# Performance work log

Hardware: AMD Instinct MI355X
Metric: run time of the kernel (lower is better)

Reference implementation:

```python
import jax, jax.numpy as jnp
import numpy as np

N = 100000
K = 16
C_IN = 64
C_MID = 64   # max(in_channels, out_channels // 2)
C_OUT = 128
EPS = 1e-5


def setup_inputs() -> dict:
    key = jax.random.key(0)
    ks = jax.random.split(key, 4)
    feat = jax.random.normal(ks[0], (N, C_IN), dtype=jnp.float32)
    reference_index = jax.random.randint(ks[1], (N, K), 0, N, dtype=jnp.int64)
    # Kaiming-ish init for the two Linear layers (torch Linear default scale)
    W1 = jax.random.normal(ks[2], (C_IN, C_MID), dtype=jnp.float32) / np.sqrt(C_IN)
    W2 = jax.random.normal(ks[3], (C_MID, C_OUT), dtype=jnp.float32) / np.sqrt(C_MID)
    return {
        "feat": feat,
        "reference_index": reference_index,
        "W1": W1,
        "b1": jnp.zeros((C_MID,), jnp.float32),
        "gamma1": jnp.ones((C_MID,), jnp.float32),
        "beta1": jnp.zeros((C_MID,), jnp.float32),
        "W2": W2,
        "b2": jnp.zeros((C_OUT,), jnp.float32),
        "gamma2": jnp.ones((C_OUT,), jnp.float32),
        "beta2": jnp.zeros((C_OUT,), jnp.float32),
    }


def _bn(x, gamma, beta):
    # BatchNorm1d in training mode: biased batch stats over the row dim.
    mean = jnp.mean(x, axis=0)
    var = jnp.var(x, axis=0)
    return (x - mean) * jax.lax.rsqrt(var + EPS) * gamma + beta


def reference(feat, reference_index, W1, b1, gamma1, beta1, W2, b2, gamma2, beta2):
    # grouping (with_xyz=False): gather neighbor features -> [N, K, C_IN]
    grouped = feat[reference_index]
    x = grouped.reshape(-1, C_IN)                 # [N*K, C_IN]
    h = jax.nn.relu(_bn(x @ W1 + b1, gamma1, beta1))   # [N*K, C_MID]
    h = jax.nn.relu(_bn(h @ W2 + b2, gamma2, beta2))   # [N*K, C_OUT]
    out = h.reshape(N, K, C_OUT).max(axis=1)      # max-pool over neighbors
    return out
```

## Files before the change

### kernel.cpp

```cpp
#include <hip/hip_runtime.h>
#include <hip/hip_bf16.h>

#define N_PTS 100000
#define KNN   16
#define NK    (N_PTS * KNN)
#define CIN   64
#define CMID  64
#define COUT  128

#define HSLC    64
#define SEG_CNT 25000
#define SEG_U32 12500

#define OFF_Z2B   0
#define OFF_Z1B   25600000
#define OFF_CNT   38400000
#define OFF_STATS 38800000
#define OFF_W2BF  38801536
#define OFF_W1BF  38817920

typedef __attribute__((ext_vector_type(8))) short bf16x8;
typedef __attribute__((ext_vector_type(4))) float f32x4;
union U8 { uint4 u; bf16x8 v; unsigned short s[8]; };

__device__ __forceinline__ unsigned short f2bf(float f) {
    unsigned u = __float_as_uint(f);
    unsigned r = (u + 0x7fffu + ((u >> 16) & 1u)) >> 16;
    return (unsigned short)r;
}

__global__ __launch_bounds__(256) void hist_k(const int* __restrict__ idx,
                                              unsigned short* __restrict__ pc) {
    __shared__ unsigned int smem[SEG_U32];
    int seg  = blockIdx.x & 3;
    int slc  = blockIdx.x >> 2;
    int base = seg * SEG_CNT;

    for (int i = threadIdx.x; i < SEG_U32; i += 256) smem[i] = 0;
    __syncthreads();

    const int4* ip = (const int4*)idx;
    const int per = NK / 4 / HSLC;
    int s = slc * per, e = s + per;
    for (int i = s + threadIdx.x; i < e; i += 256) {
        int4 v = ip[i];
        int a;
        a = v.x - base; if ((unsigned)a < (unsigned)SEG_CNT)
            atomicAdd(&smem[a >> 1], 1u << ((a & 1) * 16));
        a = v.y - base; if ((unsigned)a < (unsigned)SEG_CNT)
            atomicAdd(&smem[a >> 1], 1u << ((a & 1) * 16));
        a = v.z - base; if ((unsigned)a < (unsigned)SEG_CNT)
            atomicAdd(&smem[a >> 1], 1u << ((a & 1) * 16));
        a = v.w - base; if ((unsigned)a < (unsigned)SEG_CNT)
            atomicAdd(&smem[a >> 1], 1u << ((a & 1) * 16));
    }
    __syncthreads();

    unsigned int* outp = (unsigned int*)(pc + (size_t)slc * N_PTS) + seg * SEG_U32;
    for (int i = threadIdx.x; i < SEG_U32; i += 256) outp[i] = smem[i];
}

__global__ __launch_bounds__(256) void sum_counts_k(const unsigned short* __restrict__ pc,
                                                    float* __restrict__ counts,
                                                    const float* __restrict__ W2,
                                                    unsigned short* __restrict__ w2bf,
                                                    const float* __restrict__ W1,
                                                    unsigned short* __restrict__ w1bf) {
    if (blockIdx.x == 196) {
        for (int e = threadIdx.x; e < 8192; e += 256) {
            int j = e & 7, lane = (e >> 3) & 63, kh = (e >> 9) & 1, nt = e >> 10;
            int k = kh * 32 + (lane >> 4) * 8 + j;
            int n = nt * 16 + (lane & 15);
            w2bf[e] = f2bf(W2[k * COUT + n]);
        }
        return;
    }
    if (blockIdx.x == 197) {
        for (int e = threadIdx.x; e < 4096; e += 256) {
            int j = e & 7, lane = (e >> 3) & 63, kh = (e >> 9) & 1, nt = e >> 10;
            int k = kh * 32 + (lane >> 4) * 8 + j;
            int n = nt * 16 + (lane & 15);
            w1bf[e] = f2bf(W1[k * CMID + n]);
        }
        return;
    }
    int i = blockIdx.x * 256 + threadIdx.x;
    if (i >= N_PTS / 2) return;
    const unsigned int* p = (const unsigned int*)pc;
    unsigned int u = 0;
    #pragma unroll
    for (int s = 0; s < HSLC; s++) u += p[s * (N_PTS / 2) + i];
    float2 r;
    r.x = (float)(u & 0xffffu);
    r.y = (float)(u >> 16);
    ((float2*)counts)[i] = r;
}

__global__ __launch_bounds__(256) void gemm1_k(const float* __restrict__ feat,
                                               const unsigned short* __restrict__ w1bf,
                                               const float* __restrict__ b1,
                                               const float* __restrict__ counts,
                                               unsigned short* __restrict__ z1b,
                                               float* __restrict__ S1,
                                               float* __restrict__ Q1) {
    int lane = threadIdx.x & 63, wid = threadIdx.x >> 6;
    int il = lane & 15, quad = lane >> 4;

    bf16x8 wf[4][2];
    const uint4* wp = (const uint4*)w1bf;
    #pragma unroll
    for (int nt = 0; nt < 4; nt++) {
        U8 t0; t0.u = wp[(nt * 2 + 0) * 64 + lane]; wf[nt][0] = t0.v;
        U8 t1; t1.u = wp[(nt * 2 + 1) * 64 + lane]; wf[nt][1] = t1.v;
    }
    float bias[4];
    #pragma unroll
    for (int nt = 0; nt < 4; nt++) bias[nt] = b1[nt * 16 + il];

    float s[4] = {0, 0, 0, 0}, q[4] = {0, 0, 0, 0};

    int wgid = blockIdx.x * 4 + wid;
    for (int tile = wgid; tile < N_PTS / 16; tile += gridDim.x * 4) {
        int m0 = tile * 16;
        const float* fr = feat + (size_t)(m0 + il) * 64;
        float4 fa = *(const float4*)(fr + quad * 8);
        float4 fb = *(const float4*)(fr + quad * 8 + 4);
        float4 fc = *(const float4*)(fr + 32 + quad * 8);
        float4 fd = *(const float4*)(fr + 32 + quad * 8 + 4);
        U8 ua, ub;
        ua.s[0] = f2bf(fa.x); ua.s[1] = f2bf(fa.y); ua.s[2] = f2bf(fa.z); ua.s[3] = f2bf(fa.w);
        ua.s[4] = f2bf(fb.x); ua.s[5] = f2bf(fb.y); ua.s[6] = f2bf(fb.z); ua.s[7] = f2bf(fb.w);
        ub.s[0] = f2bf(fc.x); ub.s[1] = f2bf(fc.y); ub.s[2] = f2bf(fc.z); ub.s[3] = f2bf(fc.w);
        ub.s[4] = f2bf(fd.x); ub.s[5] = f2bf(fd.y); ub.s[6] = f2bf(fd.z); ub.s[7] = f2bf(fd.w);

        float4 cnt4 = *(const float4*)(counts + m0 + quad * 4);
        #pragma unroll
        for (int nt = 0; nt < 4; nt++) {
            f32x4 acc = {bias[nt], bias[nt], bias[nt], bias[nt]};
            acc = __builtin_amdgcn_mfma_f32_16x16x32_bf16(ua.v, wf[nt][0], acc, 0, 0, 0);
            acc = __builtin_amdgcn_mfma_f32_16x16x32_bf16(ub.v, wf[nt][1], acc, 0, 0, 0);
            unsigned short* zp = z1b + (size_t)(m0 + quad * 4) * 64 + nt * 16 + il;
            zp[0]   = f2bf(acc[0]);
            zp[64]  = f2bf(acc[1]);
            zp[128] = f2bf(acc[2]);
            zp[192] = f2bf(acc[3]);
            s[nt] += cnt4.x * acc[0] + cnt4.y * acc[1] + cnt4.z * acc[2] + cnt4.w * acc[3];
            q[nt] += cnt4.x * acc[0] * acc[0] + cnt4.y * acc[1] * acc[1]
                   + cnt4.z * acc[2] * acc[2] + cnt4.w * acc[3] * acc[3];
        }
    }
    #pragma unroll
    for (int m = 16; m <= 32; m <<= 1) {
        #pragma unroll
        for (int nt = 0; nt < 4; nt++) {
            s[nt] += __shfl_xor(s[nt], m, 64);
            q[nt] += __shfl_xor(q[nt], m, 64);
        }
    }
    __shared__ float sred[2][4][4][16];
    if (quad == 0) {
        #pragma unroll
        for (int nt = 0; nt < 4; nt++) { sred[0][wid][nt][il] = s[nt]; sred[1][wid][nt][il] = q[nt]; }
    }
    __syncthreads();
    if (threadIdx.x < 128) {
        int which = threadIdx.x >> 6, c = threadIdx.x & 63;
        float t = sred[which][0][c >> 4][c & 15] + sred[which][1][c >> 4][c & 15]
                + sred[which][2][c >> 4][c & 15] + sred[which][3][c >> 4][c & 15];
        atomicAdd(which ? &Q1[c] : &S1[c], t);
    }
}

__device__ __forceinline__ bf16x8 bnrelu(uint4 r, float4 alo, float4 ahi,
                                         float4 blo, float4 bhi) {
    float z0 = __uint_as_float(r.x << 16), z1 = __uint_as_float(r.x & 0xffff0000u);
    float z2 = __uint_as_float(r.y << 16), z3 = __uint_as_float(r.y & 0xffff0000u);
    float z4 = __uint_as_float(r.z << 16), z5 = __uint_as_float(r.z & 0xffff0000u);
    float z6 = __uint_as_float(r.w << 16), z7 = __uint_as_float(r.w & 0xffff0000u);
    U8 o;
    o.s[0] = f2bf(fmaxf(fmaf(alo.x, z0, blo.x), 0.f));
    o.s[1] = f2bf(fmaxf(fmaf(alo.y, z1, blo.y), 0.f));
    o.s[2] = f2bf(fmaxf(fmaf(alo.z, z2, blo.z), 0.f));
    o.s[3] = f2bf(fmaxf(fmaf(alo.w, z3, blo.w), 0.f));
    o.s[4] = f2bf(fmaxf(fmaf(ahi.x, z4, bhi.x), 0.f));
    o.s[5] = f2bf(fmaxf(fmaf(ahi.y, z5, bhi.y), 0.f));
    o.s[6] = f2bf(fmaxf(fmaf(ahi.z, z6, bhi.z), 0.f));
    o.s[7] = f2bf(fmaxf(fmaf(ahi.w, z7, bhi.w), 0.f));
    return o.v;
}

__global__ __launch_bounds__(256) void gemm2_k(const unsigned short* __restrict__ z1b,
                                               const unsigned short* __restrict__ w2bf,
                                               const float* __restrict__ S1,
                                               const float* __restrict__ Q1,
                                               const float* __restrict__ g1,
                                               const float* __restrict__ be1,
                                               const float* __restrict__ b2,
                                               const float* __restrict__ counts,
                                               unsigned short* __restrict__ z2b,
                                               float* __restrict__ S2,
                                               float* __restrict__ Q2) {
    __shared__ float Al[64], Bl[64];
    if (threadIdx.x < 64) {
        const float inv = 1.0f / (float)NK;
        float m = S1[threadIdx.x] * inv;
        float v = Q1[threadIdx.x] * inv - m * m;
        float a = g1[threadIdx.x] * rsqrtf(v + 1e-5f);
        Al[threadIdx.x] = a;
        Bl[threadIdx.x] = be1[threadIdx.x] - m * a;
    }
    __syncthreads();

    int lane = threadIdx.x & 63, wid = threadIdx.x >> 6;
    int il = lane & 15, quad = lane >> 4;

    float4 a0lo = *(const float4*)(Al + quad * 8);
    float4 a0hi = *(const float4*)(Al + quad * 8 + 4);
    float4 b0lo = *(const float4*)(Bl + quad * 8);
    float4 b0hi = *(const float4*)(Bl + quad * 8 + 4);
    float4 a1lo = *(const float4*)(Al + 32 + quad * 8);
    float4 a1hi = *(const float4*)(Al + 32 + quad * 8 + 4);
    float4 b1lo = *(const float4*)(Bl + 32 + quad * 8);
    float4 b1hi = *(const float4*)(Bl + 32 + quad * 8 + 4);

    bf16x8 bfr[8][2];
    const uint4* wp = (const uint4*)w2bf;
    #pragma unroll
    for (int nt = 0; nt < 8; nt++) {
        U8 t0; t0.u = wp[(nt * 2 + 0) * 64 + lane]; bfr[nt][0] = t0.v;
        U8 t1; t1.u = wp[(nt * 2 + 1) * 64 + lane]; bfr[nt][1] = t1.v;
    }
    float bias[8];
    #pragma unroll
    for (int nt = 0; nt < 8; nt++) bias[nt] = b2[nt * 16 + il];

    float s[8], q[8];
    #pragma unroll
    for (int j = 0; j < 8; j++) { s[j] = 0.f; q[j] = 0.f; }

    int wgid = blockIdx.x * 4 + wid;
    for (int tile = wgid; tile < N_PTS / 16; tile += gridDim.x * 4) {
        int m0 = tile * 16;
        const uint4* ar = (const uint4*)(z1b + (size_t)(m0 + il) * 64);
        uint4 ra0 = ar[quad];
        uint4 ra1 = ar[4 + quad];
        bf16x8 af0 = bnrelu(ra0, a0lo, a0hi, b0lo, b0hi);
        bf16x8 af1 = bnrelu(ra1, a1lo, a1hi, b1lo, b1hi);
        float4 cnt4 = *(const float4*)(counts + m0 + quad * 4);
        #pragma unroll
        for (int nt = 0; nt < 8; nt++) {
            f32x4 acc = {bias[nt], bias[nt], bias[nt], bias[nt]};
            acc = __builtin_amdgcn_mfma_f32_16x16x32_bf16(af0, bfr[nt][0], acc, 0, 0, 0);
            acc = __builtin_amdgcn_mfma_f32_16x16x32_bf16(af1, bfr[nt][1], acc, 0, 0, 0);
            unsigned short* zp = z2b + ((size_t)(nt >> 2) * N_PTS + m0 + quad * 4) * 64
                                     + (nt & 3) * 16 + il;
            zp[0]   = f2bf(acc[0]);
            zp[64]  = f2bf(acc[1]);
            zp[128] = f2bf(acc[2]);
            zp[192] = f2bf(acc[3]);
            s[nt] += cnt4.x * acc[0] + cnt4.y * acc[1] + cnt4.z * acc[2] + cnt4.w * acc[3];
            q[nt] += cnt4.x * acc[0] * acc[0] + cnt4.y * acc[1] * acc[1]
                   + cnt4.z * acc[2] * acc[2] + cnt4.w * acc[3] * acc[3];
        }
    }
    #pragma unroll
    for (int m = 16; m <= 32; m <<= 1) {
        #pragma unroll
        for (int nt = 0; nt < 8; nt++) {
            s[nt] += __shfl_xor(s[nt], m, 64);
            q[nt] += __shfl_xor(q[nt], m, 64);
        }
    }
    __shared__ float sred[2][4][8][16];
    if (quad == 0) {
        #pragma unroll
        for (int nt = 0; nt < 8; nt++) { sred[0][wid][nt][il] = s[nt]; sred[1][wid][nt][il] = q[nt]; }
    }
    __syncthreads();
    {
        int which = threadIdx.x >> 7, c = threadIdx.x & 127;
        float t = sred[which][0][c >> 4][c & 15] + sred[which][1][c >> 4][c & 15]
                + sred[which][2][c >> 4][c & 15] + sred[which][3][c >> 4][c & 15];
        atomicAdd(which ? &Q2[c] : &S2[c], t);
    }
}

__global__ __launch_bounds__(256) void gather_k(const unsigned int* __restrict__ z2u,
                                                const int* __restrict__ idx,
                                                const float* __restrict__ S2,
                                                const float* __restrict__ Q2,
                                                const float* __restrict__ g2,
                                                const float* __restrict__ be2,
                                                float* __restrict__ out) {
    int lane = threadIdx.x & 63, wid = threadIdx.x >> 6;
    int half = blockIdx.x / (N_PTS / 8);
    int n    = (blockIdx.x % (N_PTS / 8)) * 8 + wid * 2 + (lane >> 5);
    int sl   = lane & 31;

    const float inv = 1.0f / (float)NK;
    float2 Sv = ((const float2*)S2)[half * 32 + sl];
    float2 Qv = ((const float2*)Q2)[half * 32 + sl];
    float2 gv = ((const float2*)g2)[half * 32 + sl];
    float2 bv = ((const float2*)be2)[half * 32 + sl];
    float m0c = Sv.x * inv, m1c = Sv.y * inv;
    float a0 = gv.x * rsqrtf(Qv.x * inv - m0c * m0c + 1e-5f);
    float a1 = gv.y * rsqrtf(Qv.y * inv - m1c * m1c + 1e-5f);
    float b0 = bv.x - m0c * a0;
    float b1 = bv.y - m1c * a1;

    const int* ip = idx + n * KNN;
    const unsigned int* zh = z2u + (size_t)half * N_PTS * 32;
    float mx0 = -1e30f, mn0 = 1e30f, mx1 = -1e30f, mn1 = 1e30f;
    #pragma unroll
    for (int k = 0; k < KNN; k++) {
        int j = ip[k];
        unsigned v = zh[(size_t)j * 32 + sl];
        float f0 = __uint_as_float(v << 16);
        float f1 = __uint_as_float(v & 0xffff0000u);
        mx0 = fmaxf(mx0, f0); mn0 = fminf(mn0, f0);
        mx1 = fmaxf(mx1, f1); mn1 = fminf(mn1, f1);
    }
    float2 r;
    r.x = fmaxf(fmaxf(fmaf(a0, mx0, b0), fmaf(a0, mn0, b0)), 0.f);
    r.y = fmaxf(fmaxf(fmaf(a1, mx1, b1), fmaf(a1, mn1, b1)), 0.f);
    ((float2*)(out + (size_t)n * COUT + half * 64))[sl] = r;
}

extern "C" void kernel_launch(void* const* d_in, const int* in_sizes, int n_in,
                              void* d_out, int out_size, void* d_ws, size_t ws_size,
                              hipStream_t stream) {
    const float* feat = (const float*)d_in[0];
    const int*   idx  = (const int*)d_in[1];
    const float* W1   = (const float*)d_in[2];
    const float* b1   = (const float*)d_in[3];
    const float* g1   = (const float*)d_in[4];
    const float* be1  = (const float*)d_in[5];
    const float* W2   = (const float*)d_in[6];
    const float* b2   = (const float*)d_in[7];
    const float* g2   = (const float*)d_in[8];
    const float* be2  = (const float*)d_in[9];
    float* out = (float*)d_out;

    char* ws = (char*)d_ws;
    unsigned short* z2b = (unsigned short*)(ws + OFF_Z2B);
    unsigned short* pc  = (unsigned short*)(ws + OFF_Z2B);
    unsigned short* z1b = (unsigned short*)(ws + OFF_Z1B);
    float* counts = (float*)(ws + OFF_CNT);
    float* S1 = (float*)(ws + OFF_STATS);
    float* Q1 = S1 + 64;
    float* S2 = S1 + 128;
    float* Q2 = S1 + 256;
    unsigned short* w2bf = (unsigned short*)(ws + OFF_W2BF);
    unsigned short* w1bf = (unsigned short*)(ws + OFF_W1BF);

    hipMemsetAsync(ws + OFF_STATS, 0, 1536, stream);

    hist_k<<<4 * HSLC, 256, 0, stream>>>(idx, pc);
    sum_counts_k<<<198, 256, 0, stream>>>(pc, counts, W2, w2bf, W1, w1bf);
    gemm1_k<<<512, 256, 0, stream>>>(feat, w1bf, b1, counts, z1b, S1, Q1);
    gemm2_k<<<512, 256, 0, stream>>>(z1b, w2bf, S1, Q1, g1, be1, b2, counts, z2b, S2, Q2);
    gather_k<<<2 * (N_PTS / 8), 256, 0, stream>>>((const unsigned int*)z2b, idx,
                                                  S2, Q2, g2, be2, out);
}
```

Measured before the change: 206.2 us.

## Split z2 table into 16-channel slices and gather with 8 lanes per point

The gemm2 output is now laid out as eight 16-channel slices, each 32 bytes per point, instead of two 64-channel halves. The gather kernel assigns 8 threads per point per slice, loads the 16 neighbor indices as four vector nontemporal loads, and writes the output with nontemporal stores. The smaller per-slice table is meant to improve L2/MALL hit rates during the random gather and to cut per-thread index load instructions. In exchange each gather request is only 32 bytes, and gemm2 writes become narrower and more scattered.

```diff
diff --git a/kernel.cpp b/kernel.cpp
--- a/kernel.cpp
+++ b/kernel.cpp
@@ -21,6 +21,8 @@
 
 typedef __attribute__((ext_vector_type(8))) short bf16x8;
 typedef __attribute__((ext_vector_type(4))) float f32x4;
+typedef __attribute__((ext_vector_type(2))) float f32x2;
+typedef __attribute__((ext_vector_type(4))) int i32x4;
 union U8 { uint4 u; bf16x8 v; unsigned short s[8]; };
 
 __device__ __forceinline__ unsigned short f2bf(float f) {
@@ -252,12 +254,11 @@
             f32x4 acc = {bias[nt], bias[nt], bias[nt], bias[nt]};
             acc = __builtin_amdgcn_mfma_f32_16x16x32_bf16(af0, bfr[nt][0], acc, 0, 0, 0);
             acc = __builtin_amdgcn_mfma_f32_16x16x32_bf16(af1, bfr[nt][1], acc, 0, 0, 0);
-            unsigned short* zp = z2b + ((size_t)(nt >> 2) * N_PTS + m0 + quad * 4) * 64
-                                     + (nt & 3) * 16 + il;
-            zp[0]   = f2bf(acc[0]);
-            zp[64]  = f2bf(acc[1]);
-            zp[128] = f2bf(acc[2]);
-            zp[192] = f2bf(acc[3]);
+            unsigned short* zp = z2b + ((size_t)nt * N_PTS + m0 + quad * 4) * 16 + il;
+            zp[0]  = f2bf(acc[0]);
+            zp[16] = f2bf(acc[1]);
+            zp[32] = f2bf(acc[2]);
+            zp[48] = f2bf(acc[3]);
             s[nt] += cnt4.x * acc[0] + cnt4.y * acc[1] + cnt4.z * acc[2] + cnt4.w * acc[3];
             q[nt] += cnt4.x * acc[0] * acc[0] + cnt4.y * acc[1] * acc[1]
                    + cnt4.z * acc[2] * acc[2] + cnt4.w * acc[3] * acc[3];
@@ -292,38 +293,49 @@
                                                 const float* __restrict__ g2,
                                                 const float* __restrict__ be2,
                                                 float* __restrict__ out) {
-    int lane = threadIdx.x & 63, wid = threadIdx.x >> 6;
-    int half = blockIdx.x / (N_PTS / 8);
-    int n    = (blockIdx.x % (N_PTS / 8)) * 8 + wid * 2 + (lane >> 5);
-    int sl   = lane & 31;
+    int slice = blockIdx.x & 7;
+    int pblk  = blockIdx.x >> 3;
+    int grp   = threadIdx.x >> 3;
+    int sub   = threadIdx.x & 7;
+    int n     = pblk * 32 + grp;
 
     const float inv = 1.0f / (float)NK;
-    float2 Sv = ((const float2*)S2)[half * 32 + sl];
-    float2 Qv = ((const float2*)Q2)[half * 32 + sl];
-    float2 gv = ((const float2*)g2)[half * 32 + sl];
-    float2 bv = ((const float2*)be2)[half * 32 + sl];
+    float2 Sv = ((const float2*)S2)[slice * 8 + sub];
+    float2 Qv = ((const float2*)Q2)[slice * 8 + sub];
+    float2 gv = ((const float2*)g2)[slice * 8 + sub];
+    float2 bv = ((const float2*)be2)[slice * 8 + sub];
     float m0c = Sv.x * inv, m1c = Sv.y * inv;
     float a0 = gv.x * rsqrtf(Qv.x * inv - m0c * m0c + 1e-5f);
     float a1 = gv.y * rsqrtf(Qv.y * inv - m1c * m1c + 1e-5f);
     float b0 = bv.x - m0c * a0;
     float b1 = bv.y - m1c * a1;
 
-    const int* ip = idx + n * KNN;
-    const unsigned int* zh = z2u + (size_t)half * N_PTS * 32;
+    const i32x4* ip = (const i32x4*)(idx + (size_t)n * KNN);
+    i32x4 ja = __builtin_nontemporal_load(ip);
+    i32x4 jb = __builtin_nontemporal_load(ip + 1);
+    i32x4 jc = __builtin_nontemporal_load(ip + 2);
+    i32x4 jd = __builtin_nontemporal_load(ip + 3);
+
+    const unsigned int* tab = z2u + (size_t)slice * N_PTS * 8;
     float mx0 = -1e30f, mn0 = 1e30f, mx1 = -1e30f, mn1 = 1e30f;
-    #pragma unroll
-    for (int k = 0; k < KNN; k++) {
-        int j = ip[k];
-        unsigned v = zh[(size_t)j * 32 + sl];
-        float f0 = __uint_as_float(v << 16);
-        float f1 = __uint_as_float(v & 0xffff0000u);
-        mx0 = fmaxf(mx0, f0); mn0 = fminf(mn0, f0);
-        mx1 = fmaxf(mx1, f1); mn1 = fminf(mn1, f1);
-    }
-    float2 r;
-    r.x = fmaxf(fmaxf(fmaf(a0, mx0, b0), fmaf(a0, mn0, b0)), 0.f);
-    r.y = fmaxf(fmaxf(fmaf(a1, mx1, b1), fmaf(a1, mn1, b1)), 0.f);
-    ((float2*)(out + (size_t)n * COUT + half * 64))[sl] = r;
+
+#define GSTEP(J) { unsigned v = tab[(size_t)(J) * 8 + sub];                       \
+        float f0 = __uint_as_float(v << 16);                                       \
+        float f1 = __uint_as_float(v & 0xffff0000u);                               \
+        mx0 = fmaxf(mx0, f0); mn0 = fminf(mn0, f0);                                \
+        mx1 = fmaxf(mx1, f1); mn1 = fminf(mn1, f1); }
+
+    GSTEP(ja[0]); GSTEP(ja[1]); GSTEP(ja[2]); GSTEP(ja[3]);
+    GSTEP(jb[0]); GSTEP(jb[1]); GSTEP(jb[2]); GSTEP(jb[3]);
+    GSTEP(jc[0]); GSTEP(jc[1]); GSTEP(jc[2]); GSTEP(jc[3]);
+    GSTEP(jd[0]); GSTEP(jd[1]); GSTEP(jd[2]); GSTEP(jd[3]);
+#undef GSTEP
+
+    f32x2 r;
+    r[0] = fmaxf(fmaxf(fmaf(a0, mx0, b0), fmaf(a0, mn0, b0)), 0.f);
+    r[1] = fmaxf(fmaxf(fmaf(a1, mx1, b1), fmaf(a1, mn1, b1)), 0.f);
+    f32x2* op = (f32x2*)(out + (size_t)n * COUT + slice * 16);
+    __builtin_nontemporal_store(r, op + sub);
 }
 
 extern "C" void kernel_launch(void* const* d_in, const int* in_sizes, int n_in,
@@ -359,6 +371,6 @@
     sum_counts_k<<<198, 256, 0, stream>>>(pc, counts, W2, w2bf, W1, w1bf);
     gemm1_k<<<512, 256, 0, stream>>>(feat, w1bf, b1, counts, z1b, S1, Q1);
     gemm2_k<<<512, 256, 0, stream>>>(z1b, w2bf, S1, Q1, g1, be1, b2, counts, z2b, S2, Q2);
-    gather_k<<<2 * (N_PTS / 8), 256, 0, stream>>>((const unsigned int*)z2b, idx,
-                                                  S2, Q2, g2, be2, out);
-}
+    gather_k<<<8 * (N_PTS / 32), 256, 0, stream>>>((const unsigned int*)z2b, idx,
+                                                   S2, Q2, g2, be2, out);
+}
```

Result: slower. 265.1 us (+28.6%).

## Recompute second GEMM in gather kernel instead of storing z2 intermediate

Applied to the files above, without the earlier changes.

The second GEMM pass now only accumulates BN2 statistics and no longer writes the bf16 z2 buffer. A new fused kernel gathers the 16 neighbor rows of z1 per point, applies BN1+ReLU, recomputes the GEMM with MFMA, and max/min-reduces across neighbors before BN2+ReLU. This removes the z2 write and its random-gather read, which together move about 25.6 MB each way. In exchange the GEMM runs twice, once per unique point and once per neighbor, so MFMA work grows by roughly 16x.

```diff
diff --git a/kernel.cpp b/kernel.cpp
--- a/kernel.cpp
+++ b/kernel.cpp
@@ -12,7 +12,7 @@
 #define SEG_CNT 25000
 #define SEG_U32 12500
 
-#define OFF_Z2B   0
+#define OFF_PC    0
 #define OFF_Z1B   25600000
 #define OFF_CNT   38400000
 #define OFF_STATS 38800000
@@ -189,17 +189,16 @@
     return o.v;
 }
 
-__global__ __launch_bounds__(256) void gemm2_k(const unsigned short* __restrict__ z1b,
-                                               const unsigned short* __restrict__ w2bf,
-                                               const float* __restrict__ S1,
-                                               const float* __restrict__ Q1,
-                                               const float* __restrict__ g1,
-                                               const float* __restrict__ be1,
-                                               const float* __restrict__ b2,
-                                               const float* __restrict__ counts,
-                                               unsigned short* __restrict__ z2b,
-                                               float* __restrict__ S2,
-                                               float* __restrict__ Q2) {
+__global__ __launch_bounds__(256) void stats2_k(const unsigned short* __restrict__ z1b,
+                                                const unsigned short* __restrict__ w2bf,
+                                                const float* __restrict__ S1,
+                                                const float* __restrict__ Q1,
+                                                const float* __restrict__ g1,
+                                                const float* __restrict__ be1,
+                                                const float* __restrict__ b2,
+                                                const float* __restrict__ counts,
+                                                float* __restrict__ S2,
+                                                float* __restrict__ Q2) {
     __shared__ float Al[64], Bl[64];
     if (threadIdx.x < 64) {
         const float inv = 1.0f / (float)NK;
@@ -252,12 +251,6 @@
             f32x4 acc = {bias[nt], bias[nt], bias[nt], bias[nt]};
             acc = __builtin_amdgcn_mfma_f32_16x16x32_bf16(af0, bfr[nt][0], acc, 0, 0, 0);
             acc = __builtin_amdgcn_mfma_f32_16x16x32_bf16(af1, bfr[nt][1], acc, 0, 0, 0);
-            unsigned short* zp = z2b + ((size_t)(nt >> 2) * N_PTS + m0 + quad * 4) * 64
-                                     + (nt & 3) * 16 + il;
-            zp[0]   = f2bf(acc[0]);
-            zp[64]  = f2bf(acc[1]);
-            zp[128] = f2bf(acc[2]);
-            zp[192] = f2bf(acc[3]);
             s[nt] += cnt4.x * acc[0] + cnt4.y * acc[1] + cnt4.z * acc[2] + cnt4.w * acc[3];
             q[nt] += cnt4.x * acc[0] * acc[0] + cnt4.y * acc[1] * acc[1]
                    + cnt4.z * acc[2] * acc[2] + cnt4.w * acc[3] * acc[3];
@@ -285,45 +278,96 @@
     }
 }
 
-__global__ __launch_bounds__(256) void gather_k(const unsigned int* __restrict__ z2u,
-                                                const int* __restrict__ idx,
-                                                const float* __restrict__ S2,
-                                                const float* __restrict__ Q2,
-                                                const float* __restrict__ g2,
-                                                const float* __restrict__ be2,
-                                                float* __restrict__ out) {
+__global__ __launch_bounds__(256) void fused_k(const unsigned short* __restrict__ z1b,
+                                               const unsigned short* __restrict__ w2bf,
+                                               const int* __restrict__ idx,
+                                               const float* __restrict__ S1,
+                                               const float* __restrict__ Q1,
+                                               const float* __restrict__ g1,
+                                               const float* __restrict__ be1,
+                                               const float* __restrict__ b2,
+                                               const float* __restrict__ S2,
+                                               const float* __restrict__ Q2,
+                                               const float* __restrict__ g2,
+                                               const float* __restrict__ be2,
+                                               float* __restrict__ out) {
+    __shared__ float Al[64], Bl[64], A2[128], B2f[128];
+    __shared__ uint4 wlds[1024];
+
+    for (int i = threadIdx.x; i < 1024; i += 256) wlds[i] = ((const uint4*)w2bf)[i];
+    const float inv = 1.0f / (float)NK;
+    if (threadIdx.x < 64) {
+        int c = threadIdx.x;
+        float m = S1[c] * inv;
+        float v = Q1[c] * inv - m * m;
+        float a = g1[c] * rsqrtf(v + 1e-5f);
+        Al[c] = a;
+        Bl[c] = be1[c] - m * a;
+    } else if (threadIdx.x < 192) {
+        int c = threadIdx.x - 64;
+        float m = S2[c] * inv;
+        float v = Q2[c] * inv - m * m;
+        float a = g2[c] * rsqrtf(v + 1e-5f);
+        A2[c] = a;
+        B2f[c] = fmaf(a, b2[c], be2[c] - m * a);
+    }
+    __syncthreads();
+
     int lane = threadIdx.x & 63, wid = threadIdx.x >> 6;
-    int half = blockIdx.x / (N_PTS / 8);
-    int n    = (blockIdx.x % (N_PTS / 8)) * 8 + wid * 2 + (lane >> 5);
-    int sl   = lane & 31;
-
-    const float inv = 1.0f / (float)NK;
-    float2 Sv = ((const float2*)S2)[half * 32 + sl];
-    float2 Qv = ((const float2*)Q2)[half * 32 + sl];
-    float2 gv = ((const float2*)g2)[half * 32 + sl];
-    float2 bv = ((const float2*)be2)[half * 32 + sl];
-    float m0c = Sv.x * inv, m1c = Sv.y * inv;
-    float a0 = gv.x * rsqrtf(Qv.x * inv - m0c * m0c + 1e-5f);
-    float a1 = gv.y * rsqrtf(Qv.y * inv - m1c * m1c + 1e-5f);
-    float b0 = bv.x - m0c * a0;
-    float b1 = bv.y - m1c * a1;
-
-    const int* ip = idx + n * KNN;
-    const unsigned int* zh = z2u + (size_t)half * N_PTS * 32;
-    float mx0 = -1e30f, mn0 = 1e30f, mx1 = -1e30f, mn1 = 1e30f;
-    #pragma unroll
-    for (int k = 0; k < KNN; k++) {
-        int j = ip[k];
-        unsigned v = zh[(size_t)j * 32 + sl];
-        float f0 = __uint_as_float(v << 16);
-        float f1 = __uint_as_float(v & 0xffff0000u);
-        mx0 = fmaxf(mx0, f0); mn0 = fminf(mn0, f0);
-        mx1 = fmaxf(mx1, f1); mn1 = fminf(mn1, f1);
-    }
-    float2 r;
-    r.x = fmaxf(fmaxf(fmaf(a0, mx0, b0), fmaf(a0, mn0, b0)), 0.f);
-    r.y = fmaxf(fmaxf(fmaf(a1, mx1, b1), fmaf(a1, mn1, b1)), 0.f);
-    ((float2*)(out + (size_t)n * COUT + half * 64))[sl] = r;
+    int il = lane & 15, quad = lane >> 4;
+
+    float4 a0lo = *(const float4*)(Al + quad * 8);
+    float4 a0hi = *(const float4*)(Al + quad * 8 + 4);
+    float4 b0lo = *(const float4*)(Bl + quad * 8);
+    float4 b0hi = *(const float4*)(Bl + quad * 8 + 4);
+    float4 a1lo = *(const float4*)(Al + 32 + quad * 8);
+    float4 a1hi = *(const float4*)(Al + 32 + quad * 8 + 4);
+    float4 b1lo = *(const float4*)(Bl + 32 + quad * 8);
+    float4 b1hi = *(const float4*)(Bl + 32 + quad * 8 + 4);
+
+    bf16x8 bfr[8][2];
+    #pragma unroll
+    for (int nt = 0; nt < 8; nt++) {
+        U8 t0; t0.u = wlds[(nt * 2 + 0) * 64 + lane]; bfr[nt][0] = t0.v;
+        U8 t1; t1.u = wlds[(nt * 2 + 1) * 64 + lane]; bfr[nt][1] = t1.v;
+    }
+    float a2c[8], b2c[8];
+    #pragma unroll
+    for (int nt = 0; nt < 8; nt++) {
+        a2c[nt] = A2[nt * 16 + il];
+        b2c[nt] = B2f[nt * 16 + il];
+    }
+
+    int wgid = blockIdx.x * 4 + wid;
+    for (int n = wgid; n < N_PTS; n += gridDim.x * 4) {
+        int j = idx[(size_t)n * KNN + il];
+        const uint4* zr = (const uint4*)(z1b + (size_t)j * 64);
+        uint4 r0 = zr[quad];
+        uint4 r1 = zr[4 + quad];
+        bf16x8 af0 = bnrelu(r0, a0lo, a0hi, b0lo, b0hi);
+        bf16x8 af1 = bnrelu(r1, a1lo, a1hi, b1lo, b1hi);
+
+        float w0 = 0.f, w1 = 0.f;
+        #pragma unroll
+        for (int nt = 0; nt < 8; nt++) {
+            f32x4 acc = {0.f, 0.f, 0.f, 0.f};
+            acc = __builtin_amdgcn_mfma_f32_16x16x32_bf16(af0, bfr[nt][0], acc, 0, 0, 0);
+            acc = __builtin_amdgcn_mfma_f32_16x16x32_bf16(af1, bfr[nt][1], acc, 0, 0, 0);
+            float mx = fmaxf(fmaxf(acc[0], acc[1]), fmaxf(acc[2], acc[3]));
+            float mn = fminf(fminf(acc[0], acc[1]), fminf(acc[2], acc[3]));
+            mx = fmaxf(mx, __shfl_xor(mx, 16, 64));
+            mn = fminf(mn, __shfl_xor(mn, 16, 64));
+            mx = fmaxf(mx, __shfl_xor(mx, 32, 64));
+            mn = fminf(mn, __shfl_xor(mn, 32, 64));
+            float v = fmaxf(fmaxf(fmaf(a2c[nt], mx, b2c[nt]),
+                                  fmaf(a2c[nt], mn, b2c[nt])), 0.f);
+            if (nt == quad)     w0 = v;
+            if (nt == quad + 4) w1 = v;
+        }
+        float* op = out + (size_t)n * COUT;
+        op[quad * 16 + il]      = w0;
+        op[64 + quad * 16 + il] = w1;
+    }
 }
 
 extern "C" void kernel_launch(void* const* d_in, const int* in_sizes, int n_in,
@@ -342,8 +386,7 @@
     float* out = (float*)d_out;
 
     char* ws = (char*)d_ws;
-    unsigned short* z2b = (unsigned short*)(ws + OFF_Z2B);
-    unsigned short* pc  = (unsigned short*)(ws + OFF_Z2B);
+    unsigned short* pc  = (unsigned short*)(ws + OFF_PC);
     unsigned short* z1b = (unsigned short*)(ws + OFF_Z1B);
     float* counts = (float*)(ws + OFF_CNT);
     float* S1 = (float*)(ws + OFF_STATS);
@@ -358,7 +401,7 @@
     hist_k<<<4 * HSLC, 256, 0, stream>>>(idx, pc);
     sum_counts_k<<<198, 256, 0, stream>>>(pc, counts, W2, w2bf, W1, w1bf);
     gemm1_k<<<512, 256, 0, stream>>>(feat, w1bf, b1, counts, z1b, S1, Q1);
-    gemm2_k<<<512, 256, 0, stream>>>(z1b, w2bf, S1, Q1, g1, be1, b2, counts, z2b, S2, Q2);
-    gather_k<<<2 * (N_PTS / 8), 256, 0, stream>>>((const unsigned int*)z2b, idx,
-                                                  S2, Q2, g2, be2, out);
-}
+    stats2_k<<<512, 256, 0, stream>>>(z1b, w2bf, S1, Q1, g1, be1, b2, counts, S2, Q2);
+    fused_k<<<1024, 256, 0, stream>>>(z1b, w2bf, idx, S1, Q1, g1, be1, b2,
+                                      S2, Q2, g2, be2, out);
+}
```

Result: slower. 247.8 us (+20.2%).
